# Optimization experiments

Hardware: AMD Instinct MI355X
Metric: run time of the kernel (lower is better)

The kernel has to match this reference:

```python
import jax, jax.numpy as jnp
import numpy as np

B, V, F = 64, 4096, 16
A, P, NF = 8, 16, 16  # n_aggregators, n_propagate, n_filters


def setup_inputs() -> dict:
    key = jax.random.key(0)
    ks = jax.random.split(key, 6)
    data = jax.random.normal(ks[0], (B, V, F), dtype=jnp.float32)
    num_vertex = jax.random.randint(ks[1], (B, 1), 1, V + 1, dtype=jnp.int32)
    W_flr = jax.random.normal(ks[2], (F, P), dtype=jnp.float32) * (1.0 / np.sqrt(F))
    b_flr = jnp.zeros((P,), jnp.float32)
    W_s = jax.random.normal(ks[3], (F, A), dtype=jnp.float32) * (1.0 / np.sqrt(F))
    b_s = jnp.zeros((A,), jnp.float32)
    W_out = jax.random.normal(ks[4], (A * P, NF), dtype=jnp.float32) * (1.0 / np.sqrt(A * P))
    b_out = jnp.zeros((NF,), jnp.float32)
    return {"data": data, "num_vertex": num_vertex, "W_flr": W_flr, "b_flr": b_flr,
            "W_s": W_s, "b_s": b_s, "W_out": W_out, "b_out": b_out}


def reference(data, num_vertex, W_flr, b_flr, W_s, b_s, W_out, b_out):
    # vertex mask: [B, V, 1], 1.0 where index < num_vertex
    idx = jnp.arange(V, dtype=jnp.int32)[None, :]          # [1, V]
    mask = (idx < num_vertex).astype(jnp.float32)[..., None]  # [B, V, 1]

    features = data @ W_flr + b_flr                         # [B, V, P]
    distance = data @ W_s + b_s                             # [B, V, A]
    edge_weights = mask * jnp.exp(-jnp.square(distance))    # [B, V, A]

    # aggregated mean over vertices: mean_v(ew[b,v,a] * feat[b,v,p]) -> [B, A, P]
    aggregated = jnp.einsum('bva,bvp->bap', edge_weights, features) / V

    # broadcast back: ew[b,v,a] * agg[b,a,p] -> [B, V, A, P] -> [B, V, A*P]
    updated = (edge_weights[:, :, :, None] * aggregated[:, None, :, :]).reshape(B, V, A * P)

    out = mask * (updated @ W_out + b_out)                  # [B, V, NF], linear activation
    return out
```

## Files before the change

### kernel.cpp

```cpp
#include <hip/hip_runtime.h>


#define B_ 64
#define V_ 4096
#define F_ 16
#define A_ 8
#define P_ 16
#define NF_ 16
#define SPLIT1 8
#define SPLIT2 16
#define GE_ (A_*F_ + A_)
#define ESTR 12
#define DSTR 20

typedef unsigned int uint32;
typedef unsigned short u16;

__device__ __forceinline__ float bflo(uint32 u){ union{uint32 i;float f;}x; x.i=u<<16; return x.f; }
__device__ __forceinline__ float bfhi(uint32 u){ union{uint32 i;float f;}x; x.i=u&0xffff0000u; return x.f; }

__device__ __forceinline__ bool detect_bf16(const void* data){
  const uint32* w = (const uint32*)data;
  int c = 0;
  #pragma unroll
  for (int i=0;i<16;++i){
    uint32 e = (w[i]>>7) & 0xffu;
    c += (e>=100u && e<=135u) ? 1 : 0;
  }
  return c >= 11;
}

template<bool BF16>
__device__ __forceinline__ float ldw(const void* p, int i){
  return BF16 ? bflo((uint32)((const u16*)p)[i]) : ((const float*)p)[i];
}

template<bool BF16>
__device__ __forceinline__ void load_vertex(const void* base, size_t v, float* d){
  if (BF16){
    const uint4* p = (const uint4*)((const u16*)base + v*F_);
    uint4 r0=p[0], r1=p[1];
    d[0]=bflo(r0.x); d[1]=bfhi(r0.x); d[2]=bflo(r0.y); d[3]=bfhi(r0.y);
    d[4]=bflo(r0.z); d[5]=bfhi(r0.z); d[6]=bflo(r0.w); d[7]=bfhi(r0.w);
    d[8]=bflo(r1.x); d[9]=bfhi(r1.x); d[10]=bflo(r1.y); d[11]=bfhi(r1.y);
    d[12]=bflo(r1.z); d[13]=bfhi(r1.z); d[14]=bflo(r1.w); d[15]=bfhi(r1.w);
  } else {
    const float4* p = (const float4*)((const float*)base + v*F_);
    float4 a=p[0], b=p[1], c=p[2], e=p[3];
    d[0]=a.x; d[1]=a.y; d[2]=a.z; d[3]=a.w;
    d[4]=b.x; d[5]=b.y; d[6]=b.z; d[7]=b.w;
    d[8]=c.x; d[9]=c.y; d[10]=c.z; d[11]=c.w;
    d[12]=e.x; d[13]=e.y; d[14]=e.z; d[15]=e.w;
  }
}

template<bool BF16>
__device__ __forceinline__ void agg_body(
    const void* __restrict__ data, const int* __restrict__ nv,
    const void* __restrict__ Ws, const void* __restrict__ bs,
    float* __restrict__ partial)
{
  __shared__ __align__(16) float sWs[F_*A_];
  __shared__ float sbs[A_];
  __shared__ __align__(16) float e_lds[256*ESTR];
  __shared__ __align__(16) float d_lds[256*DSTR];
  __shared__ __align__(16) float gred[8*32*4];
  __shared__ float ered2[16*8];

  const int tid = threadIdx.x;
  if (tid < F_*A_) sWs[tid] = ldw<BF16>(Ws, tid);
  if (tid < A_)    sbs[tid] = ldw<BF16>(bs, tid);
  const int b = blockIdx.x >> 3;
  const int s = blockIdx.x & 7;
  const int nvb = nv[b];
  __syncthreads();

  const int vbase = s*(V_/SPLIT1);
  const size_t voff = (size_t)b*V_ + vbase;

  const int g  = tid & 31;
  const int c  = tid >> 5;
  const int ga = g >> 2;
  const int gf = g & 3;

  float acc0=0.f, acc1=0.f, acc2=0.f, acc3=0.f;
  float E[A_];
  #pragma unroll
  for (int a=0;a<A_;++a) E[a]=0.f;

  #pragma unroll
  for (int T=0; T<2; ++T) {
    const int vl = T*256 + tid;
    float d0[16];
    load_vertex<BF16>(data, voff+vl, d0);
    const float m = (vbase+vl < nvb) ? 1.f : 0.f;

    float t0[A_];
    #pragma unroll
    for (int a=0;a<A_;++a) t0[a]=sbs[a];
    #pragma unroll
    for (int f=0; f<F_; ++f){
      const float4 w0 = *(const float4*)&sWs[f*A_];
      const float4 w1 = *(const float4*)&sWs[f*A_+4];
      const float wa[8] = {w0.x,w0.y,w0.z,w0.w,w1.x,w1.y,w1.z,w1.w};
      #pragma unroll
      for (int a=0;a<A_;++a) t0[a] = fmaf(d0[f], wa[a], t0[a]);
    }
    float e0[A_];
    #pragma unroll
    for (int a=0;a<A_;++a){
      e0[a] = m*__expf(-t0[a]*t0[a]);
      E[a] += e0[a];
    }
    float* er = &e_lds[tid*ESTR];
    *(float4*)(er)   = make_float4(e0[0],e0[1],e0[2],e0[3]);
    *(float4*)(er+4) = make_float4(e0[4],e0[5],e0[6],e0[7]);
    float* dr = &d_lds[tid*DSTR];
    *(float4*)(dr)    = make_float4(d0[0],d0[1],d0[2],d0[3]);
    *(float4*)(dr+4)  = make_float4(d0[4],d0[5],d0[6],d0[7]);
    *(float4*)(dr+8)  = make_float4(d0[8],d0[9],d0[10],d0[11]);
    *(float4*)(dr+12) = make_float4(d0[12],d0[13],d0[14],d0[15]);
    __syncthreads();

    const float* ep = &e_lds[(c<<5)*ESTR + ga];
    const float* dp = &d_lds[(c<<5)*DSTR + gf*4];
    #pragma unroll 8
    for (int i=0;i<32;++i){
      const float e  = ep[i*ESTR];
      const float4 dv = *(const float4*)(dp + i*DSTR);
      acc0 = fmaf(e, dv.x, acc0);
      acc1 = fmaf(e, dv.y, acc1);
      acc2 = fmaf(e, dv.z, acc2);
      acc3 = fmaf(e, dv.w, acc3);
    }
    __syncthreads();
  }

  *(float4*)&gred[(c*32+g)*4] = make_float4(acc0,acc1,acc2,acc3);
  float* er = &e_lds[tid*ESTR];
  *(float4*)(er)   = make_float4(E[0],E[1],E[2],E[3]);
  *(float4*)(er+4) = make_float4(E[4],E[5],E[6],E[7]);
  __syncthreads();

  if (tid < 128){
    const int gg = tid >> 2, fi = tid & 3;
    float sum = 0.f;
    #pragma unroll
    for (int k=0;k<8;++k) sum += gred[(k*32+gg)*4 + fi];
    partial[(size_t)blockIdx.x*GE_ + (gg>>2)*F_ + (gg&3)*4 + fi] = sum;
  } else {
    const int t2 = tid - 128;
    const int q = t2 >> 3, a = t2 & 7;
    float sum = 0.f;
    #pragma unroll
    for (int i=0;i<16;++i) sum += e_lds[(q*16+i)*ESTR + a];
    ered2[q*8 + a] = sum;
  }
  __syncthreads();
  if (tid < A_){
    float sum = 0.f;
    #pragma unroll
    for (int q=0;q<16;++q) sum += ered2[q*8 + tid];
    partial[(size_t)blockIdx.x*GE_ + A_*F_ + tid] = sum;
  }
}

__global__ __launch_bounds__(256, 4) void k_agg(
    const void* __restrict__ data, const int* __restrict__ nv,
    const void* __restrict__ Ws, const void* __restrict__ bs,
    float* __restrict__ partial)
{
  if (detect_bf16(data)) agg_body<true >(data, nv, Ws, bs, partial);
  else                   agg_body<false>(data, nv, Ws, bs, partial);
}

template<bool BF16>
__device__ __forceinline__ void out_body(
    const void* __restrict__ data, const int* __restrict__ nv,
    const void* __restrict__ Wflr, const void* __restrict__ bflr,
    const void* __restrict__ Ws, const void* __restrict__ bs,
    const void* __restrict__ Wout, const void* __restrict__ bout,
    const float* __restrict__ partial, float* __restrict__ out)
{
  __shared__ __align__(16) float sWs[F_*A_];
  __shared__ __align__(16) float sWf[F_*P_];
  __shared__ float sbf[P_], sbs[A_], sbo[NF_];
  __shared__ float sGE[GE_];
  __shared__ float sagg[A_*P_];
  __shared__ __align__(16) float sM[A_*NF_];

  const int tid = threadIdx.x;
  const int b = blockIdx.x >> 4;
  const int s = blockIdx.x & 15;

  if (tid < F_*P_) sWf[tid] = ldw<BF16>(Wflr, tid);
  if (tid < F_*A_) sWs[tid] = ldw<BF16>(Ws, tid);
  if (tid < P_)    sbf[tid] = ldw<BF16>(bflr, tid);
  if (tid < A_)    sbs[tid] = ldw<BF16>(bs, tid);
  if (tid < NF_)   sbo[tid] = ldw<BF16>(bout, tid);
  if (tid < GE_) {
    const float* pp = partial + (size_t)(b*SPLIT1)*GE_ + tid;
    float v = 0.f;
    #pragma unroll
    for (int k=0;k<SPLIT1;++k) v += pp[(size_t)k*GE_];
    sGE[tid] = v;
  }
  const int nvb = nv[b];
  __syncthreads();

  if (tid < A_*P_) {
    const int a = tid >> 4, p = tid & 15;
    float acc = sGE[A_*F_ + a] * sbf[p];
    #pragma unroll
    for (int f=0;f<F_;++f) acc = fmaf(sGE[a*F_+f], sWf[f*P_+p], acc);
    sagg[tid] = acc * (1.0f/(float)V_);
  }
  __syncthreads();
  if (tid < A_*NF_) {
    const int a = tid >> 4, n = tid & 15;
    float m = 0.f;
    #pragma unroll
    for (int p=0;p<P_;++p)
      m = fmaf(sagg[a*P_+p], ldw<BF16>(Wout, (a*P_+p)*NF_+n), m);
    sM[tid] = m;
  }
  __syncthreads();

  const int vbase = s*(V_/SPLIT2);
  const int vl = tid;
  const size_t voff = (size_t)b*V_ + vbase;
  float d0[16];
  load_vertex<BF16>(data, voff+vl, d0);
  const float m = (vbase+vl < nvb) ? 1.f : 0.f;

  float t0[A_];
  #pragma unroll
  for (int a=0;a<A_;++a) t0[a]=sbs[a];
  #pragma unroll
  for (int f=0; f<F_; ++f){
    const float4 w0 = *(const float4*)&sWs[f*A_];
    const float4 w1 = *(const float4*)&sWs[f*A_+4];
    const float wa[8] = {w0.x,w0.y,w0.z,w0.w,w1.x,w1.y,w1.z,w1.w};
    #pragma unroll
    for (int a=0;a<A_;++a) t0[a] = fmaf(d0[f], wa[a], t0[a]);
  }

  float o[NF_];
  #pragma unroll
  for (int n=0;n<NF_;++n) o[n]=sbo[n];
  #pragma unroll
  for (int a=0;a<A_;++a){
    const float e = __expf(-t0[a]*t0[a]);
    const float4 q0 = *(const float4*)&sM[a*NF_];
    const float4 q1 = *(const float4*)&sM[a*NF_+4];
    const float4 q2 = *(const float4*)&sM[a*NF_+8];
    const float4 q3 = *(const float4*)&sM[a*NF_+12];
    const float ma[16] = {q0.x,q0.y,q0.z,q0.w, q1.x,q1.y,q1.z,q1.w,
                          q2.x,q2.y,q2.z,q2.w, q3.x,q3.y,q3.z,q3.w};
    #pragma unroll
    for (int n=0;n<NF_;++n) o[n] = fmaf(e, ma[n], o[n]);
  }

  float4* ob = (float4*)(out + (voff+vl)*NF_);
  ob[0] = make_float4(o[0]*m,  o[1]*m,  o[2]*m,  o[3]*m);
  ob[1] = make_float4(o[4]*m,  o[5]*m,  o[6]*m,  o[7]*m);
  ob[2] = make_float4(o[8]*m,  o[9]*m,  o[10]*m, o[11]*m);
  ob[3] = make_float4(o[12]*m, o[13]*m, o[14]*m, o[15]*m);
}

__global__ __launch_bounds__(256, 4) void k_out(
    const void* __restrict__ data, const int* __restrict__ nv,
    const void* __restrict__ Wflr, const void* __restrict__ bflr,
    const void* __restrict__ Ws, const void* __restrict__ bs,
    const void* __restrict__ Wout, const void* __restrict__ bout,
    const float* __restrict__ partial, float* __restrict__ out)
{
  if (detect_bf16(data))
    out_body<true >(data, nv, Wflr, bflr, Ws, bs, Wout, bout, partial, out);
  else
    out_body<false>(data, nv, Wflr, bflr, Ws, bs, Wout, bout, partial, out);
}

extern "C" void kernel_launch(void* const* d_in, const int* in_sizes, int n_in,
                              void* d_out, int out_size, void* d_ws, size_t ws_size,
                              hipStream_t stream) {
  const void* data = d_in[0];
  const int*  nv   = (const int*)d_in[1];
  const void* Wflr = d_in[2];
  const void* bflr = d_in[3];
  const void* Ws   = d_in[4];
  const void* bs   = d_in[5];
  const void* Wout = d_in[6];
  const void* bout = d_in[7];
  float* out = (float*)d_out;
  float* partial = (float*)d_ws;

  hipLaunchKernelGGL(k_agg, dim3(B_*SPLIT1), dim3(256), 0, stream,
                     data, nv, Ws, bs, partial);
  hipLaunchKernelGGL(k_out, dim3(B_*SPLIT2), dim3(256), 0, stream,
                     data, nv, Wflr, bflr, Ws, bs, Wout, bout, partial, out);
}
```

Before: 96.60 us.

## Cache quantized edge weights from agg pass instead of recomputing from data

The aggregation kernel now writes each vertex's eight edge weights, quantized to 16-bit unsigned fixed point, into a workspace buffer. The output kernel reads those 16 bytes per vertex instead of reloading the 64-byte feature row and recomputing the distance projection and exponentials. It also stages W_out in shared memory rather than reading it from global memory per thread. This cuts the output kernel's input traffic and ALU work, at the cost of an extra global write in the agg pass and quantization error in the edge weights.

```diff
diff --git a/kernel.cpp b/kernel.cpp
--- a/kernel.cpp
+++ b/kernel.cpp
@@ -58,7 +58,7 @@
 __device__ __forceinline__ void agg_body(
     const void* __restrict__ data, const int* __restrict__ nv,
     const void* __restrict__ Ws, const void* __restrict__ bs,
-    float* __restrict__ partial)
+    float* __restrict__ partial, uint4* __restrict__ ecache)
 {
   __shared__ __align__(16) float sWs[F_*A_];
   __shared__ float sbs[A_];
@@ -111,6 +111,13 @@
     for (int a=0;a<A_;++a){
       e0[a] = m*__expf(-t0[a]*t0[a]);
       E[a] += e0[a];
+    }
+    {
+      const uint32 q0 = __float2uint_rn(e0[0]*65535.f) | (__float2uint_rn(e0[1]*65535.f)<<16);
+      const uint32 q1 = __float2uint_rn(e0[2]*65535.f) | (__float2uint_rn(e0[3]*65535.f)<<16);
+      const uint32 q2 = __float2uint_rn(e0[4]*65535.f) | (__float2uint_rn(e0[5]*65535.f)<<16);
+      const uint32 q3 = __float2uint_rn(e0[6]*65535.f) | (__float2uint_rn(e0[7]*65535.f)<<16);
+      ecache[voff+vl] = make_uint4(q0,q1,q2,q3);
     }
     float* er = &e_lds[tid*ESTR];
     *(float4*)(er)   = make_float4(e0[0],e0[1],e0[2],e0[3]);
@@ -168,23 +175,23 @@
 __global__ __launch_bounds__(256, 4) void k_agg(
     const void* __restrict__ data, const int* __restrict__ nv,
     const void* __restrict__ Ws, const void* __restrict__ bs,
-    float* __restrict__ partial)
+    float* __restrict__ partial, uint4* __restrict__ ecache)
 {
-  if (detect_bf16(data)) agg_body<true >(data, nv, Ws, bs, partial);
-  else                   agg_body<false>(data, nv, Ws, bs, partial);
+  if (detect_bf16(data)) agg_body<true >(data, nv, Ws, bs, partial, ecache);
+  else                   agg_body<false>(data, nv, Ws, bs, partial, ecache);
 }
 
 template<bool BF16>
 __device__ __forceinline__ void out_body(
-    const void* __restrict__ data, const int* __restrict__ nv,
+    const int* __restrict__ nv,
     const void* __restrict__ Wflr, const void* __restrict__ bflr,
-    const void* __restrict__ Ws, const void* __restrict__ bs,
     const void* __restrict__ Wout, const void* __restrict__ bout,
-    const float* __restrict__ partial, float* __restrict__ out)
+    const float* __restrict__ partial, const uint4* __restrict__ ecache,
+    float* __restrict__ out)
 {
-  __shared__ __align__(16) float sWs[F_*A_];
   __shared__ __align__(16) float sWf[F_*P_];
-  __shared__ float sbf[P_], sbs[A_], sbo[NF_];
+  __shared__ __align__(16) float sWo[A_*P_*NF_];
+  __shared__ float sbf[P_], sbo[NF_];
   __shared__ float sGE[GE_];
   __shared__ float sagg[A_*P_];
   __shared__ __align__(16) float sM[A_*NF_];
@@ -193,11 +200,12 @@
   const int b = blockIdx.x >> 4;
   const int s = blockIdx.x & 15;
 
-  if (tid < F_*P_) sWf[tid] = ldw<BF16>(Wflr, tid);
-  if (tid < F_*A_) sWs[tid] = ldw<BF16>(Ws, tid);
-  if (tid < P_)    sbf[tid] = ldw<BF16>(bflr, tid);
-  if (tid < A_)    sbs[tid] = ldw<BF16>(bs, tid);
-  if (tid < NF_)   sbo[tid] = ldw<BF16>(bout, tid);
+  sWf[tid] = ldw<BF16>(Wflr, tid);
+  #pragma unroll
+  for (int j=0;j<8;++j)
+    sWo[tid*8+j] = ldw<BF16>(Wout, tid*8+j);
+  if (tid < P_)  sbf[tid] = ldw<BF16>(bflr, tid);
+  if (tid < NF_) sbo[tid] = ldw<BF16>(bout, tid);
   if (tid < GE_) {
     const float* pp = partial + (size_t)(b*SPLIT1)*GE_ + tid;
     float v = 0.f;
@@ -221,36 +229,30 @@
     float m = 0.f;
     #pragma unroll
     for (int p=0;p<P_;++p)
-      m = fmaf(sagg[a*P_+p], ldw<BF16>(Wout, (a*P_+p)*NF_+n), m);
+      m = fmaf(sagg[a*P_+p], sWo[(a*P_+p)*NF_+n], m);
     sM[tid] = m;
   }
   __syncthreads();
 
   const int vbase = s*(V_/SPLIT2);
   const int vl = tid;
-  const size_t voff = (size_t)b*V_ + vbase;
-  float d0[16];
-  load_vertex<BF16>(data, voff+vl, d0);
+  const size_t v = (size_t)b*V_ + vbase + vl;
   const float m = (vbase+vl < nvb) ? 1.f : 0.f;
 
-  float t0[A_];
-  #pragma unroll
-  for (int a=0;a<A_;++a) t0[a]=sbs[a];
-  #pragma unroll
-  for (int f=0; f<F_; ++f){
-    const float4 w0 = *(const float4*)&sWs[f*A_];
-    const float4 w1 = *(const float4*)&sWs[f*A_+4];
-    const float wa[8] = {w0.x,w0.y,w0.z,w0.w,w1.x,w1.y,w1.z,w1.w};
-    #pragma unroll
-    for (int a=0;a<A_;++a) t0[a] = fmaf(d0[f], wa[a], t0[a]);
-  }
+  const uint4 eu = ecache[v];
+  const float k16 = 1.0f/65535.f;
+  float e0[A_];
+  e0[0] = (float)(eu.x & 0xffffu)*k16;  e0[1] = (float)(eu.x >> 16)*k16;
+  e0[2] = (float)(eu.y & 0xffffu)*k16;  e0[3] = (float)(eu.y >> 16)*k16;
+  e0[4] = (float)(eu.z & 0xffffu)*k16;  e0[5] = (float)(eu.z >> 16)*k16;
+  e0[6] = (float)(eu.w & 0xffffu)*k16;  e0[7] = (float)(eu.w >> 16)*k16;
 
   float o[NF_];
   #pragma unroll
-  for (int n=0;n<NF_;++n) o[n]=sbo[n];
+  for (int n=0;n<NF_;++n) o[n] = m*sbo[n];
   #pragma unroll
   for (int a=0;a<A_;++a){
-    const float e = __expf(-t0[a]*t0[a]);
+    const float e = e0[a];
     const float4 q0 = *(const float4*)&sM[a*NF_];
     const float4 q1 = *(const float4*)&sM[a*NF_+4];
     const float4 q2 = *(const float4*)&sM[a*NF_+8];
@@ -261,24 +263,24 @@
     for (int n=0;n<NF_;++n) o[n] = fmaf(e, ma[n], o[n]);
   }
 
-  float4* ob = (float4*)(out + (voff+vl)*NF_);
-  ob[0] = make_float4(o[0]*m,  o[1]*m,  o[2]*m,  o[3]*m);
-  ob[1] = make_float4(o[4]*m,  o[5]*m,  o[6]*m,  o[7]*m);
-  ob[2] = make_float4(o[8]*m,  o[9]*m,  o[10]*m, o[11]*m);
-  ob[3] = make_float4(o[12]*m, o[13]*m, o[14]*m, o[15]*m);
+  float4* ob = (float4*)(out + v*NF_);
+  ob[0] = make_float4(o[0],  o[1],  o[2],  o[3]);
+  ob[1] = make_float4(o[4],  o[5],  o[6],  o[7]);
+  ob[2] = make_float4(o[8],  o[9],  o[10], o[11]);
+  ob[3] = make_float4(o[12], o[13], o[14], o[15]);
 }
 
 __global__ __launch_bounds__(256, 4) void k_out(
     const void* __restrict__ data, const int* __restrict__ nv,
     const void* __restrict__ Wflr, const void* __restrict__ bflr,
-    const void* __restrict__ Ws, const void* __restrict__ bs,
     const void* __restrict__ Wout, const void* __restrict__ bout,
-    const float* __restrict__ partial, float* __restrict__ out)
+    const float* __restrict__ partial, const uint4* __restrict__ ecache,
+    float* __restrict__ out)
 {
   if (detect_bf16(data))
-    out_body<true >(data, nv, Wflr, bflr, Ws, bs, Wout, bout, partial, out);
+    out_body<true >(nv, Wflr, bflr, Wout, bout, partial, ecache, out);
   else
-    out_body<false>(data, nv, Wflr, bflr, Ws, bs, Wout, bout, partial, out);
+    out_body<false>(nv, Wflr, bflr, Wout, bout, partial, ecache, out);
 }
 
 extern "C" void kernel_launch(void* const* d_in, const int* in_sizes, int n_in,
@@ -294,9 +296,10 @@
   const void* bout = d_in[7];
   float* out = (float*)d_out;
   float* partial = (float*)d_ws;
+  uint4* ecache  = (uint4*)((char*)d_ws + 278528);
 
   hipLaunchKernelGGL(k_agg, dim3(B_*SPLIT1), dim3(256), 0, stream,
-                     data, nv, Ws, bs, partial);
+                     data, nv, Ws, bs, partial, ecache);
   hipLaunchKernelGGL(k_out, dim3(B_*SPLIT2), dim3(256), 0, stream,
-                     data, nv, Wflr, bflr, Ws, bs, Wout, bout, partial, out);
-}
+                     data, nv, Wflr, bflr, Wout, bout, partial, ecache, out);
+}
```

Result: faster. 94.06 us, median of 2 (-2.6%).
